# Performance work log

Hardware: AMD Instinct MI355X
Metric: run time of the kernel (lower is better)

Reference implementation:

```python
import jax, jax.numpy as jnp
import numpy as np

V = 100000          # vocab size
D = 256             # hidden dim
B, N = 32, 128      # batch, max_len
K = 100             # noise_ratio
NORM_TERM = 11.512925  # log(V), norm_term='auto'
BACKOFF_PROB = 1e-10


def setup_inputs() -> dict:
    key = jax.random.key(0)
    ks = jax.random.split(key, 6)
    target = jax.random.randint(ks[0], (B, N), 0, V)
    noise_samples = jax.random.randint(ks[1], (B, N, K), 0, V)
    hidden = jax.random.normal(ks[2], (B, N, D), dtype=jnp.float32) * 0.1
    weight = jax.random.normal(ks[3], (V, D), dtype=jnp.float32) * 0.05
    bias = jax.random.normal(ks[4], (V,), dtype=jnp.float32) * 0.01
    u = jax.random.uniform(ks[5], (V,), dtype=jnp.float32) + BACKOFF_PROB
    noise_probs = u / jnp.sum(u)  # normalized noise distribution
    return {"target": target, "noise_samples": noise_samples, "hidden": hidden,
            "weight": weight, "bias": bias, "noise_probs": noise_probs}


def reference(target, noise_samples, hidden, weight, bias, noise_probs):
    # score_noise = log P_noise(noise_samples)   (B,N,K) -- irregular gather on (V,)
    score_noise = jnp.log(noise_probs)[noise_samples]
    # get_score (IndexLinear): gathered output-embedding dot products
    w_t = weight[target]                                   # (B,N,D)
    score_model = jnp.einsum('bnd,bnd->bn', hidden, w_t) + bias[target] - NORM_TERM
    w_n = weight[noise_samples]                            # (B,N,K,D) big gather
    score_noise_in_model = (jnp.einsum('bnd,bnkd->bnk', hidden, w_n)
                            + bias[noise_samples] - NORM_TERM)
    # NCE binary classification loss (score_target_in_noise passed as zeros)
    log_k = jnp.log(jnp.float32(K))
    logit_true = score_model - log_k                        # (B,N) label=1
    logit_noise = score_noise_in_model - score_noise - log_k  # (B,N,K) label=0
    # BCE-with-logits: -log sigmoid(x) = softplus(-x); -log(1-sigmoid(x)) = softplus(x)
    loss = jax.nn.softplus(-logit_true) + jnp.sum(jax.nn.softplus(logit_noise), axis=-1)
    # reduction='elementwise_mean'
    return jnp.mean(loss)
```

## Files before the change

kernel.cpp:

```cpp
#include <hip/hip_runtime.h>
#include <math.h>

#define V 100000
#define D 256
#define B 32
#define N 128
#define K 100
#define NPOS (B * N)
#define NPAIR (NPOS * (K + 1))
#define BIN_ROWS 32
#define NBIN (V / BIN_ROWS)
#define NSHARD 16
#define CAP_S 32
#define MAXTOT (NSHARD * CAP_S)
#define GRIDC 1024
#define BPB 4
#define ROW_W32 136
#define HVEC (NPOS * D / 4)
#define NORM_TERM 11.512925f
#define LOG_K 4.605170186f

typedef float    f32x4 __attribute__((ext_vector_type(4)));
typedef unsigned u32x2 __attribute__((ext_vector_type(2)));
typedef unsigned u32x4 __attribute__((ext_vector_type(4)));
typedef __fp16   f16x2 __attribute__((ext_vector_type(2)));

__device__ __forceinline__ float softplus(float x) {
    return fmaxf(x, 0.f) + __logf(1.f + __expf(-fabsf(x)));
}

__device__ __forceinline__ unsigned pack_f16(float a, float b) {
#if __has_builtin(__builtin_amdgcn_cvt_pkrtz)
    f16x2 h = __builtin_amdgcn_cvt_pkrtz(a, b);
#else
    f16x2 h; h.x = (__fp16)a; h.y = (__fp16)b;
#endif
    union { f16x2 h; unsigned u; } c; c.h = h;
    return c.u;
}

#if __has_builtin(__builtin_amdgcn_fdot2)
#define DOT2(a, b, c) __builtin_amdgcn_fdot2((a), (b), (c), false)
#else
__device__ __forceinline__ float DOT2(f16x2 a, f16x2 b, float c) {
    return fmaf((float)a.x, (float)b.x, fmaf((float)a.y, (float)b.y, c));
}
#endif

union V4H { u32x4 u; f16x2 h[4]; };

template <int CTRL>
__device__ __forceinline__ float dpp_add(float x) {
    int y = __builtin_amdgcn_update_dpp(__float_as_int(x), __float_as_int(x),
                                        CTRL, 0xF, 0xF, false);
    return x + __int_as_float(y);
}
__device__ __forceinline__ float quarter_sum(float x) {
    x = dpp_add<0xB1>(x);
    x = dpp_add<0x4E>(x);
    x = dpp_add<0x141>(x);
    x = dpp_add<0x140>(x);
    return x;
}

__global__ __launch_bounds__(256) void scatter_hconv_kernel(
    const int* __restrict__ target, const int* __restrict__ noise,
    const float* __restrict__ hidden,
    int* __restrict__ cursor, unsigned* __restrict__ buf,
    unsigned* __restrict__ htab32)
{
    const int p = blockIdx.x * 256 + threadIdx.x;

    int row, pos; unsigned flag;
    if (p < NPOS * K) { pos = p / K; row = noise[p]; flag = 0u; }
    else              { pos = p - NPOS * K; row = target[pos]; flag = 1u; }
    const int cell = (row >> 5) * NSHARD + (blockIdx.x & (NSHARD - 1));
    const int slot = atomicAdd(&cursor[cell], 1);
    if (slot < CAP_S)
        buf[(size_t)cell * CAP_S + slot] =
            ((unsigned)(row & (BIN_ROWS - 1)) << 13) | ((unsigned)pos << 1) | flag;

    if (p < HVEC) {
        const f32x4 h4 = *((const f32x4*)hidden + p);
        u32x2 o;
        o.x = pack_f16(h4.x, h4.y);
        o.y = pack_f16(h4.z, h4.w);
        *(u32x2*)(htab32 + (size_t)p * 2) = o;
    }
}

__global__ __launch_bounds__(256, 4) void compute_kernel(
    const unsigned* __restrict__ htab32, const float* __restrict__ weight,
    const float* __restrict__ bias, const float* __restrict__ noise_probs,
    const int* __restrict__ cursor, const unsigned* __restrict__ buf,
    float* __restrict__ out)
{
    __shared__ unsigned slab32[BIN_ROWS * ROW_W32];
    __shared__ float    sbias[BPB * BIN_ROWS];
    __shared__ float    slogp[BPB * BIN_ROWS];
    __shared__ unsigned plist[MAXTOT];
    __shared__ int      scnt[BPB * NSHARD];
    __shared__ int      pref[BPB][NSHARD + 1];
    __shared__ float    wsum[4];

    const int b0  = blockIdx.x;
    const int tid = threadIdx.x;
    const int wave = tid >> 6;
    const int lane = tid & 63;
    const int q    = lane >> 4;
    const int ql   = lane & 15;

    if (tid < BPB * NSHARD) {
        const int j = tid >> 4, s = tid & 15, bin = b0 + j * GRIDC;
        scnt[tid] = (bin < NBIN) ? min(cursor[bin * NSHARD + s], CAP_S) : 0;
    }
    __syncthreads();
    if (tid < BPB) {
        int s = 0;
        #pragma unroll
        for (int i = 0; i < NSHARD; ++i) { pref[tid][i] = s; s += scnt[tid * NSHARD + i]; }
        pref[tid][NSHARD] = s;
    }
    __syncthreads();

    for (int r = wave; r < BIN_ROWS; r += 4) {
        const f32x4 w4 = __builtin_nontemporal_load(
            (const f32x4*)(weight + (size_t)(b0 * BIN_ROWS + r) * D + lane * 4));
        u32x2 o;
        o.x = pack_f16(w4.x, w4.y);
        o.y = pack_f16(w4.z, w4.w);
        *(u32x2*)(slab32 + r * ROW_W32 + lane * 2) = o;
    }
    if (tid < BPB * BIN_ROWS) {
        const int j = tid >> 5, r = tid & 31, bin = b0 + j * GRIDC;
        if (bin < NBIN) {
            sbias[tid] = bias[bin * BIN_ROWS + r];
            slogp[tid] = __logf(noise_probs[bin * BIN_ROWS + r]);
        }
    }
    {
        const int total0 = pref[0][NSHARD];
        for (int i = tid; i < total0; i += 256) {
            int s = 0;
            #pragma unroll
            for (int m = 1; m < NSHARD; ++m) s += (i >= pref[0][m]);
            plist[i] = buf[((size_t)(b0 * NSHARD + s)) * CAP_S + (i - pref[0][s])];
        }
    }
    __syncthreads();

    float loss = 0.f;
    for (int j = 0; j < BPB; ++j) {
        const int bin   = b0 + j * GRIDC;
        const int total = (bin < NBIN) ? pref[j][NSHARD] : 0;
        const int bin_n = bin + GRIDC;
        const bool hasnext = (j + 1 < BPB) && (bin_n < NBIN);

        f32x4 wpre[8];
        if (hasnext) {
            const float* wsrc = weight + (size_t)bin_n * BIN_ROWS * D;
            #pragma unroll
            for (int i = 0; i < 8; ++i)
                wpre[i] = __builtin_nontemporal_load(
                    (const f32x4*)(wsrc + (size_t)(wave + 4 * i) * D + lane * 4));
        }
        unsigned pl_a = 0u, pl_b = 0u; int tot_n = 0;
        if (hasnext) {
            tot_n = pref[j + 1][NSHARD];
            if (tid < tot_n) {
                int s = 0;
                #pragma unroll
                for (int m = 1; m < NSHARD; ++m) s += (tid >= pref[j + 1][m]);
                pl_a = buf[((size_t)(bin_n * NSHARD + s)) * CAP_S + (tid - pref[j + 1][s])];
            }
            if (tid + 256 < tot_n) {
                int s = 0;
                #pragma unroll
                for (int m = 1; m < NSHARD; ++m) s += (tid + 256 >= pref[j + 1][m]);
                pl_b = buf[((size_t)(bin_n * NSHARD + s)) * CAP_S + (tid + 256 - pref[j + 1][s])];
            }
        }

        {
            const int p0 = wave * 4 + q;
            unsigned rec_c = (p0 < total) ? plist[p0] : 0u;
            V4H H0c, H1c;
            {
                const u32x4* hp = (const u32x4*)(htab32
                    + (size_t)((rec_c >> 1) & (NPOS - 1)) * 128) + ql;
                H0c.u = hp[0];
                H1c.u = hp[16];
            }
            for (int base = wave * 4; base < total; base += 16) {
                const int p = base + q;
                const int pn = p + 16;
                const unsigned rec_n = (pn < total) ? plist[pn] : 0u;
                const u32x4* hpn = (const u32x4*)(htab32
                    + (size_t)((rec_n >> 1) & (NPOS - 1)) * 128) + ql;
                V4H H0n, H1n;
                H0n.u = hpn[0];
                H1n.u = hpn[16];

                const int rloc = (int)((rec_c >> 13) & (BIN_ROWS - 1));
                const unsigned* wr = slab32 + rloc * ROW_W32;
                V4H W0, W1;
                W0.u = *(const u32x4*)(wr + ql * 4);
                W1.u = *(const u32x4*)(wr + 64 + ql * 4);

                float a0 = 0.f, a1 = 0.f, a2 = 0.f, a3 = 0.f;
                a0 = DOT2(H0c.h[0], W0.h[0], a0);
                a1 = DOT2(H0c.h[1], W0.h[1], a1);
                a2 = DOT2(H0c.h[2], W0.h[2], a2);
                a3 = DOT2(H0c.h[3], W0.h[3], a3);
                a0 = DOT2(H1c.h[0], W1.h[0], a0);
                a1 = DOT2(H1c.h[1], W1.h[1], a1);
                a2 = DOT2(H1c.h[2], W1.h[2], a2);
                a3 = DOT2(H1c.h[3], W1.h[3], a3);

                const float r = quarter_sum((a0 + a1) + (a2 + a3));

                const float score = r + sbias[j * BIN_ROWS + rloc] - NORM_TERM;
                const float x = (rec_c & 1u) ? (LOG_K - score)
                                             : (score - slogp[j * BIN_ROWS + rloc] - LOG_K);
                if ((p < total) && ql == 0) loss += softplus(x);

                rec_c = rec_n;
                H0c = H0n;
                H1c = H1n;
            }
        }
        __syncthreads();

        if (hasnext) {
            #pragma unroll
            for (int i = 0; i < 8; ++i) {
                u32x2 o;
                o.x = pack_f16(wpre[i].x, wpre[i].y);
                o.y = pack_f16(wpre[i].z, wpre[i].w);
                *(u32x2*)(slab32 + (wave + 4 * i) * ROW_W32 + lane * 2) = o;
            }
            if (tid < tot_n)       plist[tid]       = pl_a;
            if (tid + 256 < tot_n) plist[tid + 256] = pl_b;
        }
        __syncthreads();
    }

    loss += __shfl_xor(loss, 16, 64);
    loss += __shfl_xor(loss, 32, 64);
    if (lane == 0) wsum[wave] = loss;
    __syncthreads();
    if (tid == 0)
        atomicAdd(out, (wsum[0] + wsum[1] + wsum[2] + wsum[3])
                       * (1.0f / (float)NPOS));
}

extern "C" void kernel_launch(void* const* d_in, const int* in_sizes, int n_in,
                              void* d_out, int out_size, void* d_ws, size_t ws_size,
                              hipStream_t stream) {
    const int*   target      = (const int*)d_in[0];
    const int*   noise       = (const int*)d_in[1];
    const float* hidden      = (const float*)d_in[2];
    const float* weight      = (const float*)d_in[3];
    const float* bias        = (const float*)d_in[4];
    const float* noise_probs = (const float*)d_in[5];
    float* out = (float*)d_out;

    const size_t cursor_bytes = (size_t)NBIN * NSHARD * 4;
    const size_t buf_bytes    = (size_t)NBIN * NSHARD * CAP_S * 4;
    int*      cursor = (int*)d_ws;
    unsigned* buf    = (unsigned*)((char*)d_ws + cursor_bytes);
    unsigned* htab32 = (unsigned*)((char*)d_ws + cursor_bytes + buf_bytes);

    (void)hipMemsetAsync(cursor, 0, cursor_bytes, stream);
    (void)hipMemsetAsync(out, 0, sizeof(float), stream);

    scatter_hconv_kernel<<<NPAIR / 256, 256, 0, stream>>>(
        target, noise, hidden, cursor, buf, htab32);
    compute_kernel<<<GRIDC, 256, 0, stream>>>(
        htab32, weight, bias, noise_probs, cursor, buf, out);
}
```

Measured before the change: 198.9 us.

## Fuse scatter and compute into one cooperative kernel with grid sync

Merges the scatter/hidden-conversion kernel and the compute kernel into a single cooperative-launch kernel separated by a grid-wide sync. Before the sync, each block prefetches its first two weight bins so those loads overlap the scatter phase, which also saves a kernel launch. It falls back to the two-kernel path if cooperative launch or occupancy of 4 blocks per CU is unavailable. The grid barrier adds its own sync cost, and higher register pressure from the prefetch buffers may limit occupancy.

```diff
diff --git a/kernel.cpp b/kernel.cpp
--- a/kernel.cpp
+++ b/kernel.cpp
@@ -1,4 +1,5 @@
 #include <hip/hip_runtime.h>
+#include <hip/hip_cooperative_groups.h>
 #include <math.h>
 
 #define V 100000
@@ -20,6 +21,8 @@
 #define NORM_TERM 11.512925f
 #define LOG_K 4.605170186f
 
+namespace cg = cooperative_groups;
+
 typedef float    f32x4 __attribute__((ext_vector_type(4)));
 typedef unsigned u32x2 __attribute__((ext_vector_type(2)));
 typedef unsigned u32x4 __attribute__((ext_vector_type(4)));
@@ -61,6 +64,213 @@
     x = dpp_add<0x141>(x);
     x = dpp_add<0x140>(x);
     return x;
+}
+
+__global__ __launch_bounds__(256, 4) void fused_kernel(
+    const int* __restrict__ target, const int* __restrict__ noise,
+    const float* __restrict__ hidden, const float* __restrict__ weight,
+    const float* __restrict__ bias, const float* __restrict__ noise_probs,
+    int* __restrict__ cursor, unsigned* __restrict__ buf,
+    unsigned* __restrict__ htab32, float* __restrict__ out)
+{
+    __shared__ unsigned slab32[BIN_ROWS * ROW_W32];
+    __shared__ float    sbias[BPB * BIN_ROWS];
+    __shared__ float    slogp[BPB * BIN_ROWS];
+    __shared__ unsigned plist[MAXTOT];
+    __shared__ int      scnt[BPB * NSHARD];
+    __shared__ int      pref[BPB][NSHARD + 1];
+    __shared__ float    wsum[4];
+
+    const int b0   = blockIdx.x;
+    const int tid  = threadIdx.x;
+    const int wave = tid >> 6;
+    const int lane = tid & 63;
+    const int q    = lane >> 4;
+    const int ql   = lane & 15;
+
+    f32x4 w0pre[8], wpre[8];
+    {
+        const float* w0 = weight + (size_t)b0 * BIN_ROWS * D;
+        const float* w1 = weight + (size_t)(b0 + GRIDC) * BIN_ROWS * D;
+        #pragma unroll
+        for (int i = 0; i < 8; ++i)
+            w0pre[i] = __builtin_nontemporal_load(
+                (const f32x4*)(w0 + (size_t)(wave + 4 * i) * D + lane * 4));
+        #pragma unroll
+        for (int i = 0; i < 8; ++i)
+            wpre[i] = __builtin_nontemporal_load(
+                (const f32x4*)(w1 + (size_t)(wave + 4 * i) * D + lane * 4));
+    }
+    asm volatile("" ::: "memory");
+
+    if (tid < BPB * BIN_ROWS) {
+        const int j = tid >> 5, r = tid & 31, bin = b0 + j * GRIDC;
+        if (bin < NBIN) {
+            sbias[tid] = bias[bin * BIN_ROWS + r];
+            slogp[tid] = __logf(noise_probs[bin * BIN_ROWS + r]);
+        }
+    }
+
+    for (int p = b0 * 256 + tid; p < NPAIR; p += GRIDC * 256) {
+        int row, pos; unsigned flag;
+        if (p < NPOS * K) { pos = p / K; row = noise[p]; flag = 0u; }
+        else              { pos = p - NPOS * K; row = target[pos]; flag = 1u; }
+        const int cell = (row >> 5) * NSHARD + (b0 & (NSHARD - 1));
+        const int slot = atomicAdd(&cursor[cell], 1);
+        if (slot < CAP_S)
+            buf[(size_t)cell * CAP_S + slot] =
+                ((unsigned)(row & (BIN_ROWS - 1)) << 13) | ((unsigned)pos << 1) | flag;
+    }
+
+    {
+        const int p2 = b0 * 256 + tid;
+        const f32x4 h4 = *((const f32x4*)hidden + p2);
+        u32x2 o;
+        o.x = pack_f16(h4.x, h4.y);
+        o.y = pack_f16(h4.z, h4.w);
+        *(u32x2*)(htab32 + (size_t)p2 * 2) = o;
+    }
+
+    if (b0 == 0 && tid == 0) *out = 0.f;
+
+    #pragma unroll
+    for (int i = 0; i < 8; ++i) {
+        u32x2 o;
+        o.x = pack_f16(w0pre[i].x, w0pre[i].y);
+        o.y = pack_f16(w0pre[i].z, w0pre[i].w);
+        *(u32x2*)(slab32 + (wave + 4 * i) * ROW_W32 + lane * 2) = o;
+    }
+
+    __threadfence();
+    cg::this_grid().sync();
+    __threadfence();
+
+    if (tid < BPB * NSHARD) {
+        const int j = tid >> 4, s = tid & 15, bin = b0 + j * GRIDC;
+        scnt[tid] = (bin < NBIN) ? min(cursor[bin * NSHARD + s], CAP_S) : 0;
+    }
+    __syncthreads();
+    if (tid < BPB) {
+        int s = 0;
+        #pragma unroll
+        for (int i = 0; i < NSHARD; ++i) { pref[tid][i] = s; s += scnt[tid * NSHARD + i]; }
+        pref[tid][NSHARD] = s;
+    }
+    __syncthreads();
+
+    {
+        const int total0 = pref[0][NSHARD];
+        for (int i = tid; i < total0; i += 256) {
+            int s = 0;
+            #pragma unroll
+            for (int m = 1; m < NSHARD; ++m) s += (i >= pref[0][m]);
+            plist[i] = buf[((size_t)(b0 * NSHARD + s)) * CAP_S + (i - pref[0][s])];
+        }
+    }
+    __syncthreads();
+
+    float loss = 0.f;
+    for (int j = 0; j < BPB; ++j) {
+        const int bin   = b0 + j * GRIDC;
+        const int total = (bin < NBIN) ? pref[j][NSHARD] : 0;
+        const int bin_n = bin + GRIDC;
+        const bool hasnext = (j + 1 < BPB) && (bin_n < NBIN);
+
+        if (hasnext && j > 0) {
+            const float* wsrc = weight + (size_t)bin_n * BIN_ROWS * D;
+            #pragma unroll
+            for (int i = 0; i < 8; ++i)
+                wpre[i] = __builtin_nontemporal_load(
+                    (const f32x4*)(wsrc + (size_t)(wave + 4 * i) * D + lane * 4));
+        }
+        unsigned pl_a = 0u, pl_b = 0u; int tot_n = 0;
+        if (hasnext) {
+            tot_n = pref[j + 1][NSHARD];
+            if (tid < tot_n) {
+                int s = 0;
+                #pragma unroll
+                for (int m = 1; m < NSHARD; ++m) s += (tid >= pref[j + 1][m]);
+                pl_a = buf[((size_t)(bin_n * NSHARD + s)) * CAP_S + (tid - pref[j + 1][s])];
+            }
+            if (tid + 256 < tot_n) {
+                int s = 0;
+                #pragma unroll
+                for (int m = 1; m < NSHARD; ++m) s += (tid + 256 >= pref[j + 1][m]);
+                pl_b = buf[((size_t)(bin_n * NSHARD + s)) * CAP_S + (tid + 256 - pref[j + 1][s])];
+            }
+        }
+
+        {
+            const int p0 = wave * 4 + q;
+            unsigned rec_c = (p0 < total) ? plist[p0] : 0u;
+            V4H H0c, H1c;
+            {
+                const u32x4* hp = (const u32x4*)(htab32
+                    + (size_t)((rec_c >> 1) & (NPOS - 1)) * 128) + ql;
+                H0c.u = hp[0];
+                H1c.u = hp[16];
+            }
+            for (int base = wave * 4; base < total; base += 16) {
+                const int p = base + q;
+                const int pn = p + 16;
+                const unsigned rec_n = (pn < total) ? plist[pn] : 0u;
+                const u32x4* hpn = (const u32x4*)(htab32
+                    + (size_t)((rec_n >> 1) & (NPOS - 1)) * 128) + ql;
+                V4H H0n, H1n;
+                H0n.u = hpn[0];
+                H1n.u = hpn[16];
+
+                const int rloc = (int)((rec_c >> 13) & (BIN_ROWS - 1));
+                const unsigned* wr = slab32 + rloc * ROW_W32;
+                V4H W0, W1;
+                W0.u = *(const u32x4*)(wr + ql * 4);
+                W1.u = *(const u32x4*)(wr + 64 + ql * 4);
+
+                float a0 = 0.f, a1 = 0.f, a2 = 0.f, a3 = 0.f;
+                a0 = DOT2(H0c.h[0], W0.h[0], a0);
+                a1 = DOT2(H0c.h[1], W0.h[1], a1);
+                a2 = DOT2(H0c.h[2], W0.h[2], a2);
+                a3 = DOT2(H0c.h[3], W0.h[3], a3);
+                a0 = DOT2(H1c.h[0], W1.h[0], a0);
+                a1 = DOT2(H1c.h[1], W1.h[1], a1);
+                a2 = DOT2(H1c.h[2], W1.h[2], a2);
+                a3 = DOT2(H1c.h[3], W1.h[3], a3);
+
+                const float r = quarter_sum((a0 + a1) + (a2 + a3));
+
+                const float score = r + sbias[j * BIN_ROWS + rloc] - NORM_TERM;
+                const float x = (rec_c & 1u) ? (LOG_K - score)
+                                             : (score - slogp[j * BIN_ROWS + rloc] - LOG_K);
+                if ((p < total) && ql == 0) loss += softplus(x);
+
+                rec_c = rec_n;
+                H0c = H0n;
+                H1c = H1n;
+            }
+        }
+        __syncthreads();
+
+        if (hasnext) {
+            #pragma unroll
+            for (int i = 0; i < 8; ++i) {
+                u32x2 o;
+                o.x = pack_f16(wpre[i].x, wpre[i].y);
+                o.y = pack_f16(wpre[i].z, wpre[i].w);
+                *(u32x2*)(slab32 + (wave + 4 * i) * ROW_W32 + lane * 2) = o;
+            }
+            if (tid < tot_n)       plist[tid]       = pl_a;
+            if (tid + 256 < tot_n) plist[tid + 256] = pl_b;
+        }
+        __syncthreads();
+    }
+
+    loss += __shfl_xor(loss, 16, 64);
+    loss += __shfl_xor(loss, 32, 64);
+    if (lane == 0) wsum[wave] = loss;
+    __syncthreads();
+    if (tid == 0)
+        atomicAdd(out, (wsum[0] + wsum[1] + wsum[2] + wsum[3])
+                       * (1.0f / (float)NPOS));
 }
 
 __global__ __launch_bounds__(256) void scatter_hconv_kernel(
@@ -271,9 +481,33 @@
     unsigned* buf    = (unsigned*)((char*)d_ws + cursor_bytes);
     unsigned* htab32 = (unsigned*)((char*)d_ws + cursor_bytes + buf_bytes);
 
+    static int mode = -1;
+    if (mode < 0) {
+        int dev = 0;
+        (void)hipGetDevice(&dev);
+        int coopAttr = 0;
+        if (hipDeviceGetAttribute(&coopAttr, hipDeviceAttributeCooperativeLaunch,
+                                  dev) != hipSuccess) coopAttr = 0;
+        int maxb = 0;
+        hipError_t oe = hipOccupancyMaxActiveBlocksPerMultiprocessor(
+            &maxb, fused_kernel, 256, 0);
+        mode = (coopAttr && oe == hipSuccess && maxb >= 4) ? 1 : 0;
+    }
+
     (void)hipMemsetAsync(cursor, 0, cursor_bytes, stream);
+
+    if (mode == 1) {
+        void* args[] = { (void*)&target, (void*)&noise, (void*)&hidden,
+                         (void*)&weight, (void*)&bias, (void*)&noise_probs,
+                         (void*)&cursor, (void*)&buf, (void*)&htab32,
+                         (void*)&out };
+        hipError_t e = hipLaunchCooperativeKernel(
+            (const void*)fused_kernel, dim3(GRIDC), dim3(256), args, 0, stream);
+        if (e == hipSuccess) return;
+        mode = 0;
+    }
+
     (void)hipMemsetAsync(out, 0, sizeof(float), stream);
-
     scatter_hconv_kernel<<<NPAIR / 256, 256, 0, stream>>>(
         target, noise, hidden, cursor, buf, htab32);
     compute_kernel<<<GRIDC, 256, 0, stream>>>(
```

After: 200.4 us. No clear change (+0.7%).
